# Performance work log

Measured on AMD Instinct MI355X. Metric: run time of the kernel, lower is better.

## Reference

```python
import jax, jax.numpy as jnp
import numpy as np

B, XD, PD, D, H = 512, 32768, 512, 64, 128  # batch, x_dim, proj_dim, latent_dim, per_dim_hidden
G1 = 1024  # gene projector hidden (hardcoded in module)


def _init(k, shape, fan_in):
    s = 1.0 / np.sqrt(fan_in)
    return jax.random.uniform(k, shape, jnp.float32, -s, s)


def setup_inputs() -> dict:
    key = jax.random.key(0)
    ks = jax.random.split(key, 16)
    return {
        "x": jax.random.normal(ks[0], (B, XD), jnp.float32),
        "z": jax.random.normal(ks[1], (B, D), jnp.float32),
        "perm": jax.random.permutation(ks[2], B).astype(jnp.int32),
        # shared gene projector
        "Wg1": _init(ks[3], (XD, G1), XD), "bg1": _init(ks[4], (G1,), XD),
        "Wg2": _init(ks[5], (G1, PD), G1), "bg2": _init(ks[6], (PD,), G1),
        # per-dimension 3-layer MLPs, stacked over D. Layer-1 weight [PD+1, H]
        # is split into the h-part Wh and the z-part Wz (last input column).
        "Wh": _init(ks[7], (D, PD, H), PD + 1),
        "Wz": _init(ks[8], (D, H), PD + 1),
        "b1": _init(ks[9], (D, H), PD + 1),
        "W2": _init(ks[10], (D, H, H), H), "b2": _init(ks[11], (D, H), H),
        "W3": _init(ks[12], (D, H), H), "b3": _init(ks[13], (D,), H),
    }


def reference(x, z, perm, Wg1, bg1, Wg2, bg2, Wh, Wz, b1, W2, b2, W3, b3):
    elu = jax.nn.elu
    # shared gene projector (eval mode: dropout = identity, no noise)
    h = elu(elu(x @ Wg1 + bg1) @ Wg2 + bg2)            # [B, PD]
    # batched layer-1 of all D per-dim nets; h-projection computed once and
    # reused for the marginal pass via permutation (h_shuffled = h[perm]).
    hWh = jnp.einsum('bp,dph->bdh', h, Wh)             # [B, D, H]
    zWz = z[:, :, None] * Wz[None]                     # [B, D, H]

    def head(a1_pre):
        a1 = elu(a1_pre)                               # [B, D, H]
        a2 = elu(jnp.einsum('bdh,dhk->bdk', a1, W2) + b2)
        return jnp.einsum('bdh,dh->bd', a2, W3) + b3   # [B, D] scalar scores

    joint_score = head(hWh + zWz + b1)                 # T(h, z_j)
    marg_score = head(hWh[perm] + zWz + b1)            # T(h_shuffled, z_j)

    emas = jnp.ones((D,), x.dtype)                     # buffer init = ones, eval: no update
    et = jnp.mean(jnp.exp(marg_score), axis=0)         # [D]
    mi = jnp.mean(joint_score, axis=0) - jnp.log(et / emas)
    return -jnp.mean(mi)
```

## Files before the change

### kernel.cpp

```cpp
#include <hip/hip_runtime.h>
#include <hip/hip_bf16.h>
#include <math.h>

#define B_  512
#define XD_ 32768
#define PD_ 512
#define D_  64
#define H_  128
#define G1_ 1024

typedef __attribute__((ext_vector_type(8))) short short8v;
typedef __attribute__((ext_vector_type(4))) float floatx4;

__device__ __forceinline__ float eluf(float v) { return v > 0.f ? v : expm1f(v); }

__device__ __forceinline__ void split8t(const float* c, short8v& h, short8v& l) {
    unsigned hu[8], lu[8];
    #pragma unroll
    for (int j = 0; j < 8; j++) {
        unsigned u = __float_as_uint(c[j]);
        hu[j] = u & 0xFFFF0000u;
        float res = c[j] - __uint_as_float(hu[j]);
        lu[j] = __float_as_uint(res);
    }
    uint4 hp, lp;
    hp.x = __builtin_amdgcn_perm(hu[1], hu[0], 0x07060302u);
    hp.y = __builtin_amdgcn_perm(hu[3], hu[2], 0x07060302u);
    hp.z = __builtin_amdgcn_perm(hu[5], hu[4], 0x07060302u);
    hp.w = __builtin_amdgcn_perm(hu[7], hu[6], 0x07060302u);
    lp.x = __builtin_amdgcn_perm(lu[1], lu[0], 0x07060302u);
    lp.y = __builtin_amdgcn_perm(lu[3], lu[2], 0x07060302u);
    lp.z = __builtin_amdgcn_perm(lu[5], lu[4], 0x07060302u);
    lp.w = __builtin_amdgcn_perm(lu[7], lu[6], 0x07060302u);
    h = __builtin_bit_cast(short8v, hp);
    l = __builtin_bit_cast(short8v, lp);
}

__global__ __launch_bounds__(256) void k_tr(const float* __restrict__ x,
                                            float* __restrict__ xT) {
    __shared__ float tile[64][65];
    const int k0 = blockIdx.x * 64;
    const int m0 = blockIdx.y * 64;
    const int t = threadIdx.x;
    const int tk = t & 63, tg = t >> 6;
    #pragma unroll
    for (int i = 0; i < 16; i++) {
        int r = tg * 16 + i;
        tile[r][tk] = x[(size_t)(m0 + r) * XD_ + k0 + tk];
    }
    __syncthreads();
    #pragma unroll
    for (int i = 0; i < 16; i++) {
        int r = tg * 16 + i;
        xT[(size_t)(k0 + r) * B_ + m0 + tk] = tile[tk][r];
    }
}

__global__ __launch_bounds__(256, 2) void k_gemm1t(const float* __restrict__ xT,
                                                   const float* __restrict__ Wg1,
                                                   float* __restrict__ part,
                                                   int KS) {
    __shared__ ushort Ah[2][4 * 128 * 8], Al[2][4 * 128 * 8];
    __shared__ ushort Bh[2][4 * 128 * 8], Bl[2][4 * 128 * 8];
    const int nt = blockIdx.x, mt = blockIdx.y, ks = blockIdx.z;
    const int t = threadIdx.x;
    const int w = t >> 6, lane = t & 63;
    const int q = lane >> 4, l15 = lane & 15;
    const int wr = w >> 1, wc = w & 1;
    const int kbS = t >> 6, pr = t & 63;
    const int k0 = ks * KS;

    const float* Ag = xT + (size_t)(k0 + kbS * 8) * B_ + mt * 128 + pr * 2;
    const float* Bg = Wg1 + (size_t)(k0 + kbS * 8) * G1_ + nt * 128 + pr * 2;

    floatx4 acc[4][4];
    #pragma unroll
    for (int i = 0; i < 4; i++)
        #pragma unroll
        for (int j = 0; j < 4; j++) acc[i][j] = (floatx4){0.f, 0.f, 0.f, 0.f};

    float2 pa[8], pb[8];
    #pragma unroll
    for (int kk = 0; kk < 8; kk++) {
        pa[kk] = *(const float2*)(Ag + (size_t)kk * B_);
        pb[kk] = *(const float2*)(Bg + (size_t)kk * G1_);
    }

    auto stage = [&](int buf) {
        float a0[8], a1[8], c0[8], c1[8];
        #pragma unroll
        for (int kk = 0; kk < 8; kk++) {
            a0[kk] = pa[kk].x; a1[kk] = pa[kk].y;
            c0[kk] = pb[kk].x; c1[kk] = pb[kk].y;
        }
        short8v ah0, al0, ah1, al1, bh0, bl0, bh1, bl1;
        split8t(a0, ah0, al0); split8t(a1, ah1, al1);
        split8t(c0, bh0, bl0); split8t(c1, bh1, bl1);
        int n0 = pr * 2;
        int ia0 = (kbS * 128 + (n0 ^ kbS)) * 8;
        int ia1 = (kbS * 128 + ((n0 + 1) ^ kbS)) * 8;
        *(short8v*)&Ah[buf][ia0] = ah0; *(short8v*)&Al[buf][ia0] = al0;
        *(short8v*)&Ah[buf][ia1] = ah1; *(short8v*)&Al[buf][ia1] = al1;
        *(short8v*)&Bh[buf][ia0] = bh0; *(short8v*)&Bl[buf][ia0] = bl0;
        *(short8v*)&Bh[buf][ia1] = bh1; *(short8v*)&Bl[buf][ia1] = bl1;
    };

    auto mma = [&](int buf) {
        short8v af[4], alf[4], bf[4], blf[4];
        #pragma unroll
        for (int i = 0; i < 4; i++) {
            int m = wr * 64 + i * 16 + l15;
            int idx = (q * 128 + (m ^ q)) * 8;
            af[i]  = *(const short8v*)&Ah[buf][idx];
            alf[i] = *(const short8v*)&Al[buf][idx];
        }
        #pragma unroll
        for (int j = 0; j < 4; j++) {
            int n = wc * 64 + j * 16 + l15;
            int idx = (q * 128 + (n ^ q)) * 8;
            bf[j]  = *(const short8v*)&Bh[buf][idx];
            blf[j] = *(const short8v*)&Bl[buf][idx];
        }
        #pragma unroll
        for (int i = 0; i < 4; i++)
            #pragma unroll
            for (int j = 0; j < 4; j++) {
                acc[i][j] = __builtin_amdgcn_mfma_f32_16x16x32_bf16(af[i],  bf[j],  acc[i][j], 0, 0, 0);
                acc[i][j] = __builtin_amdgcn_mfma_f32_16x16x32_bf16(af[i],  blf[j], acc[i][j], 0, 0, 0);
                acc[i][j] = __builtin_amdgcn_mfma_f32_16x16x32_bf16(alf[i], bf[j],  acc[i][j], 0, 0, 0);
            }
    };

    stage(0);
    #pragma unroll
    for (int kk = 0; kk < 8; kk++) {
        pa[kk] = *(const float2*)(Ag + (size_t)(32 + kk) * B_);
        pb[kk] = *(const float2*)(Bg + (size_t)(32 + kk) * G1_);
    }
    asm volatile("s_waitcnt lgkmcnt(0)" ::: "memory");
    __builtin_amdgcn_s_barrier();

    const int NT = KS >> 5;
    for (int it = 0; it < NT - 1; it++) {
        const int cur = it & 1;
        stage(cur ^ 1);
        if (it + 2 < NT) {
            #pragma unroll
            for (int kk = 0; kk < 8; kk++) {
                pa[kk] = *(const float2*)(Ag + (size_t)((it + 2) * 32 + kk) * B_);
                pb[kk] = *(const float2*)(Bg + (size_t)((it + 2) * 32 + kk) * G1_);
            }
        }
        mma(cur);
        asm volatile("s_waitcnt lgkmcnt(0)" ::: "memory");
        __builtin_amdgcn_s_barrier();
    }
    mma((NT - 1) & 1);

    float* P = part + (size_t)ks * (B_ * G1_) + (size_t)(mt * 128) * G1_ + nt * 128;
    #pragma unroll
    for (int i = 0; i < 4; i++)
        #pragma unroll
        for (int j = 0; j < 4; j++) {
            int col = wc * 64 + j * 16 + l15;
            #pragma unroll
            for (int r = 0; r < 4; r++) {
                int row = wr * 64 + i * 16 + q * 4 + r;
                P[(size_t)row * G1_ + col] = acc[i][j][r];
            }
        }
}

__global__ __launch_bounds__(256, 2) void k_gemm1m(const float* __restrict__ x,
                                                   const float* __restrict__ Wg1,
                                                   float* __restrict__ part,
                                                   int KS) {
    __shared__ ushort Ah[4 * 128 * 8], Al[4 * 128 * 8];
    __shared__ ushort Bh[4 * 128 * 8], Bl[4 * 128 * 8];
    const int nt = blockIdx.x, mt = blockIdx.y, ks = blockIdx.z;
    const int t = threadIdx.x;
    const int w = t >> 6, lane = t & 63;
    const int q = lane >> 4, l15 = lane & 15;
    const int wr = w >> 1, wc = w & 1;
    const int kbB = t >> 6, nb = t & 63;
    const int mA = t & 127, kbA = t >> 7;
    const int k0 = ks * KS;

    const float* Ag = x + (size_t)(mt * 128 + mA) * XD_ + k0 + kbA * 8;
    const float* Bg = Wg1 + (size_t)(k0 + kbB * 8) * G1_ + nt * 128 + nb * 2;

    floatx4 acc[4][4];
    #pragma unroll
    for (int i = 0; i < 4; i++)
        #pragma unroll
        for (int j = 0; j < 4; j++) acc[i][j] = (floatx4){0.f, 0.f, 0.f, 0.f};

    float4 pa0 = *(const float4*)(Ag);
    float4 pa1 = *(const float4*)(Ag + 4);
    float4 pa2 = *(const float4*)(Ag + 16);
    float4 pa3 = *(const float4*)(Ag + 20);
    float2 pb[8];
    #pragma unroll
    for (int kk = 0; kk < 8; kk++) pb[kk] = *(const float2*)(Bg + (size_t)kk * G1_);

    for (int kt = 0; kt < KS; kt += 32) {
        float cA0[8] = {pa0.x, pa0.y, pa0.z, pa0.w, pa1.x, pa1.y, pa1.z, pa1.w};
        float cA1[8] = {pa2.x, pa2.y, pa2.z, pa2.w, pa3.x, pa3.y, pa3.z, pa3.w};
        float c0[8], c1[8];
        #pragma unroll
        for (int kk = 0; kk < 8; kk++) { c0[kk] = pb[kk].x; c1[kk] = pb[kk].y; }
        short8v ah0, al0, ah1, al1, bh0, bl0, bh1, bl1;
        split8t(cA0, ah0, al0);
        split8t(cA1, ah1, al1);
        split8t(c0, bh0, bl0);
        split8t(c1, bh1, bl1);
        if (kt + 32 < KS) {
            pa0 = *(const float4*)(Ag + kt + 32);
            pa1 = *(const float4*)(Ag + kt + 36);
            pa2 = *(const float4*)(Ag + kt + 48);
            pa3 = *(const float4*)(Ag + kt + 52);
            const float* p = Bg + (size_t)(kt + 32) * G1_;
            #pragma unroll
            for (int kk = 0; kk < 8; kk++) pb[kk] = *(const float2*)(p + (size_t)kk * G1_);
        }
        {
            int ia0 = (kbA * 128 + (mA ^ kbA)) * 8;
            int ia1 = ((kbA + 2) * 128 + (mA ^ (kbA + 2))) * 8;
            *(short8v*)&Ah[ia0] = ah0; *(short8v*)&Al[ia0] = al0;
            *(short8v*)&Ah[ia1] = ah1; *(short8v*)&Al[ia1] = al1;
            int n0i = nb * 2;
            int i0 = (kbB * 128 + (n0i ^ kbB)) * 8;
            int i1 = (kbB * 128 + ((n0i + 1) ^ kbB)) * 8;
            *(short8v*)&Bh[i0] = bh0; *(short8v*)&Bl[i0] = bl0;
            *(short8v*)&Bh[i1] = bh1; *(short8v*)&Bl[i1] = bl1;
        }
        __syncthreads();
        short8v af[4], alf[4], bf[4], blf[4];
        #pragma unroll
        for (int i = 0; i < 4; i++) {
            int m = wr * 64 + i * 16 + l15;
            int idx = (q * 128 + (m ^ q)) * 8;
            af[i]  = *(const short8v*)&Ah[idx];
            alf[i] = *(const short8v*)&Al[idx];
        }
        #pragma unroll
        for (int j = 0; j < 4; j++) {
            int n = wc * 64 + j * 16 + l15;
            int idx = (q * 128 + (n ^ q)) * 8;
            bf[j]  = *(const short8v*)&Bh[idx];
            blf[j] = *(const short8v*)&Bl[idx];
        }
        #pragma unroll
        for (int i = 0; i < 4; i++)
            #pragma unroll
            for (int j = 0; j < 4; j++) {
                acc[i][j] = __builtin_amdgcn_mfma_f32_16x16x32_bf16(af[i],  bf[j],  acc[i][j], 0, 0, 0);
                acc[i][j] = __builtin_amdgcn_mfma_f32_16x16x32_bf16(af[i],  blf[j], acc[i][j], 0, 0, 0);
                acc[i][j] = __builtin_amdgcn_mfma_f32_16x16x32_bf16(alf[i], bf[j],  acc[i][j], 0, 0, 0);
            }
        __syncthreads();
    }
    float* P = part + (size_t)ks * (B_ * G1_) + (size_t)(mt * 128) * G1_ + nt * 128;
    #pragma unroll
    for (int i = 0; i < 4; i++)
        #pragma unroll
        for (int j = 0; j < 4; j++) {
            int col = wc * 64 + j * 16 + l15;
            #pragma unroll
            for (int r = 0; r < 4; r++) {
                int row = wr * 64 + i * 16 + q * 4 + r;
                P[(size_t)row * G1_ + col] = acc[i][j][r];
            }
        }
}

__global__ __launch_bounds__(256) void k_red1(const float* __restrict__ part,
                                              const float* __restrict__ bg1,
                                              ushort* __restrict__ Gh,
                                              ushort* __restrict__ Gl,
                                              int nparts) {
    int idx = (blockIdx.x * 256 + threadIdx.x) * 8;
    const int S = B_ * G1_;
    float c[8] = {};
    for (int k = 0; k < nparts; k++) {
        const float* p = part + (size_t)k * S + idx;
        float4 v0 = *(const float4*)p, v1 = *(const float4*)(p + 4);
        c[0] += v0.x; c[1] += v0.y; c[2] += v0.z; c[3] += v0.w;
        c[4] += v1.x; c[5] += v1.y; c[6] += v1.z; c[7] += v1.w;
    }
    int cb = idx & (G1_ - 1);
    float4 b0 = *(const float4*)(bg1 + cb), b1v = *(const float4*)(bg1 + cb + 4);
    c[0] = eluf(c[0] + b0.x); c[1] = eluf(c[1] + b0.y);
    c[2] = eluf(c[2] + b0.z); c[3] = eluf(c[3] + b0.w);
    c[4] = eluf(c[4] + b1v.x); c[5] = eluf(c[5] + b1v.y);
    c[6] = eluf(c[6] + b1v.z); c[7] = eluf(c[7] + b1v.w);
    short8v h, l; split8t(c, h, l);
    *(short8v*)(Gh + idx) = h;
    *(short8v*)(Gl + idx) = l;
}

__global__ __launch_bounds__(256, 2) void k_gemm2m(const ushort* __restrict__ Gh,
                                                   const ushort* __restrict__ Gl,
                                                   const float* __restrict__ Wg2,
                                                   float* __restrict__ part2) {
    __shared__ ushort Ah[4 * 64 * 8], Al[4 * 64 * 8];
    __shared__ ushort Bh[4 * 64 * 8], Bl[4 * 64 * 8];
    const int nt = blockIdx.x, mt = blockIdx.y, ks = blockIdx.z;
    const int t = threadIdx.x;
    const int w = t >> 6, lane = t & 63;
    const int q = lane >> 4, l15 = lane & 15;
    const int kb = (t >> 4) & 3;
    const int rb = (t & 15) | (w << 4);
    const int k0 = ks * 128;

    const int cB = t & 63, g = t >> 6;

    floatx4 acc[4];
    #pragma unroll
    for (int i = 0; i < 4; i++) acc[i] = (floatx4){0.f, 0.f, 0.f, 0.f};

    for (int kt = 0; kt < 128; kt += 32) {
        {
            const ushort* pH = Gh + (size_t)(mt * 64 + rb) * G1_ + k0 + kt + kb * 8;
            const ushort* pL = Gl + (size_t)(mt * 64 + rb) * G1_ + k0 + kt + kb * 8;
            uint4 vh = *(const uint4*)pH;
            uint4 vl = *(const uint4*)pL;
            int idx = (kb * 64 + (rb ^ kb)) * 8;
            *(uint4*)&Ah[idx] = vh;
            *(uint4*)&Al[idx] = vl;
        }
        {
            float c[8];
            const float* p = Wg2 + (size_t)(k0 + kt + g * 8) * PD_ + nt * 64 + cB;
            #pragma unroll
            for (int kk = 0; kk < 8; kk++) c[kk] = p[(size_t)kk * PD_];
            short8v h, l; split8t(c, h, l);
            int idx = (g * 64 + (cB ^ g)) * 8;
            *(short8v*)&Bh[idx] = h;
            *(short8v*)&Bl[idx] = l;
        }
        __syncthreads();
        short8v af[4], alf[4], bf, blf;
        #pragma unroll
        for (int i = 0; i < 4; i++) {
            int m = i * 16 + l15;
            int idx = (q * 64 + (m ^ q)) * 8;
            af[i]  = *(const short8v*)&Ah[idx];
            alf[i] = *(const short8v*)&Al[idx];
        }
        {
            int n = w * 16 + l15;
            int idx = (q * 64 + (n ^ q)) * 8;
            bf  = *(const short8v*)&Bh[idx];
            blf = *(const short8v*)&Bl[idx];
        }
        #pragma unroll
        for (int i = 0; i < 4; i++) {
            acc[i] = __builtin_amdgcn_mfma_f32_16x16x32_bf16(af[i],  bf,  acc[i], 0, 0, 0);
            acc[i] = __builtin_amdgcn_mfma_f32_16x16x32_bf16(af[i],  blf, acc[i], 0, 0, 0);
            acc[i] = __builtin_amdgcn_mfma_f32_16x16x32_bf16(alf[i], bf,  acc[i], 0, 0, 0);
        }
        __syncthreads();
    }
    float* P = part2 + (size_t)ks * (B_ * PD_) + (size_t)(mt * 64) * PD_ + nt * 64;
    #pragma unroll
    for (int i = 0; i < 4; i++) {
        int col = w * 16 + l15;
        #pragma unroll
        for (int r = 0; r < 4; r++) {
            int row = i * 16 + q * 4 + r;
            P[(size_t)row * PD_ + col] = acc[i][r];
        }
    }
}

__global__ __launch_bounds__(256) void k_red2(const float* __restrict__ part2,
                                              const float* __restrict__ bg2,
                                              ushort* __restrict__ hh,
                                              ushort* __restrict__ hl) {
    int idx = (blockIdx.x * 256 + threadIdx.x) * 8;
    const int S = B_ * PD_;
    float c[8] = {};
    #pragma unroll
    for (int k = 0; k < 8; k++) {
        const float* p = part2 + (size_t)k * S + idx;
        float4 v0 = *(const float4*)p, v1 = *(const float4*)(p + 4);
        c[0] += v0.x; c[1] += v0.y; c[2] += v0.z; c[3] += v0.w;
        c[4] += v1.x; c[5] += v1.y; c[6] += v1.z; c[7] += v1.w;
    }
    int cb = idx & (PD_ - 1);
    float4 b0 = *(const float4*)(bg2 + cb), b1v = *(const float4*)(bg2 + cb + 4);
    c[0] = eluf(c[0] + b0.x); c[1] = eluf(c[1] + b0.y);
    c[2] = eluf(c[2] + b0.z); c[3] = eluf(c[3] + b0.w);
    c[4] = eluf(c[4] + b1v.x); c[5] = eluf(c[5] + b1v.y);
    c[6] = eluf(c[6] + b1v.z); c[7] = eluf(c[7] + b1v.w);
    short8v h, l; split8t(c, h, l);
    *(short8v*)(hh + idx) = h;
    *(short8v*)(hl + idx) = l;
}

__global__ __launch_bounds__(256, 2) void k_hwh_m(const ushort* __restrict__ hh,
                                                  const ushort* __restrict__ hl,
                                                  const float* __restrict__ Wh,
                                                  float* __restrict__ hWh) {
    __shared__ ushort Ah[4 * 64 * 8], Al[4 * 64 * 8];
    __shared__ ushort Bh[4 * 128 * 8], Bl[4 * 128 * 8];
    const int d = blockIdx.x, mt = blockIdx.y;
    const int t = threadIdx.x;
    const int w = t >> 6, lane = t & 63;
    const int q = lane >> 4, l15 = lane & 15;
    const int kb = (t >> 4) & 3;
    const int rb = (t & 15) | (w << 4);

    const ushort* AgH = hh + (size_t)(mt * 64 + rb) * PD_ + kb * 8;
    const ushort* AgL = hl + (size_t)(mt * 64 + rb) * PD_ + kb * 8;
    const float* Bg = Wh + (size_t)d * (PD_ * H_) + (size_t)(kb * 8) * H_ + rb * 2;

    floatx4 acc[4][2];
    #pragma unroll
    for (int i = 0; i < 4; i++)
        #pragma unroll
        for (int j = 0; j < 2; j++) acc[i][j] = (floatx4){0.f, 0.f, 0.f, 0.f};

    uint4 pah = *(const uint4*)(AgH);
    uint4 pal = *(const uint4*)(AgL);
    float2 pb[8];
    #pragma unroll
    for (int kk = 0; kk < 8; kk++) pb[kk] = *(const float2*)(Bg + (size_t)kk * H_);

    for (int kt = 0; kt < PD_; kt += 32) {
        float c0[8], c1[8];
        #pragma unroll
        for (int kk = 0; kk < 8; kk++) { c0[kk] = pb[kk].x; c1[kk] = pb[kk].y; }
        short8v bh0, bl0, bh1, bl1;
        split8t(c0, bh0, bl0);
        split8t(c1, bh1, bl1);
        uint4 ah = pah, al = pal;
        if (kt + 32 < PD_) {
            pah = *(const uint4*)(AgH + kt + 32);
            pal = *(const uint4*)(AgL + kt + 32);
            const float* p = Bg + (size_t)(kt + 32) * H_;
            #pragma unroll
            for (int kk = 0; kk < 8; kk++) pb[kk] = *(const float2*)(p + (size_t)kk * H_);
        }
        {
            int idx = (kb * 64 + (rb ^ kb)) * 8;
            *(uint4*)&Ah[idx] = ah;
            *(uint4*)&Al[idx] = al;
            int n0i = rb * 2;
            int i0 = (kb * 128 + (n0i ^ kb)) * 8;
            int i1 = (kb * 128 + ((n0i + 1) ^ kb)) * 8;
            *(short8v*)&Bh[i0] = bh0; *(short8v*)&Bl[i0] = bl0;
            *(short8v*)&Bh[i1] = bh1; *(short8v*)&Bl[i1] = bl1;
        }
        __syncthreads();
        short8v af[4], alf[4], bf[2], blf[2];
        #pragma unroll
        for (int i = 0; i < 4; i++) {
            int m = i * 16 + l15;
            int idx = (q * 64 + (m ^ q)) * 8;
            af[i]  = *(const short8v*)&Ah[idx];
            alf[i] = *(const short8v*)&Al[idx];
        }
        #pragma unroll
        for (int j = 0; j < 2; j++) {
            int n = w * 32 + j * 16 + l15;
            int idx = (q * 128 + (n ^ q)) * 8;
            bf[j]  = *(const short8v*)&Bh[idx];
            blf[j] = *(const short8v*)&Bl[idx];
        }
        #pragma unroll
        for (int i = 0; i < 4; i++)
            #pragma unroll
            for (int j = 0; j < 2; j++) {
                acc[i][j] = __builtin_amdgcn_mfma_f32_16x16x32_bf16(af[i],  bf[j],  acc[i][j], 0, 0, 0);
                acc[i][j] = __builtin_amdgcn_mfma_f32_16x16x32_bf16(af[i],  blf[j], acc[i][j], 0, 0, 0);
                acc[i][j] = __builtin_amdgcn_mfma_f32_16x16x32_bf16(alf[i], bf[j],  acc[i][j], 0, 0, 0);
            }
        __syncthreads();
    }
    #pragma unroll
    for (int i = 0; i < 4; i++)
        #pragma unroll
        for (int j = 0; j < 2; j++) {
            int col = w * 32 + j * 16 + l15;
            #pragma unroll
            for (int r = 0; r < 4; r++) {
                int row = i * 16 + q * 4 + r;
                int b = mt * 64 + row;
                hWh[(size_t)b * (D_ * H_) + d * H_ + col] = acc[i][j][r];
            }
        }
}

__global__ __launch_bounds__(256, 2) void k_heads(const float* __restrict__ hWh,
                                                  const float* __restrict__ z,
                                                  const int* __restrict__ perm,
                                                  const float* __restrict__ Wz,
                                                  const float* __restrict__ b1,
                                                  const float* __restrict__ W2,
                                                  const float* __restrict__ b2,
                                                  const float* __restrict__ W3,
                                                  const float* __restrict__ b3,
                                                  float* __restrict__ jpart,
                                                  float* __restrict__ epart) {
    const int chunk = blockIdx.x;
    const int d = blockIdx.y;
    const int t = threadIdx.x;
    const int b0 = chunk * 64;
    __shared__ ushort A1h[16 * 64 * 8];
    __shared__ ushort A1l[16 * 64 * 8];
    __shared__ float  BS[4096];
    ushort* Bh = (ushort*)BS;
    ushort* Bl = Bh + 4096;
    float*  sred = BS;

    const int w = t >> 6, lane = t & 63;
    const int q = lane >> 4, l15 = lane & 15;
    const int kb = (t >> 4) & 3;
    const int rb = (t & 15) | (w << 4);

    const float* W2d = W2 + (size_t)d * H_ * H_;
    const float* Wzd = Wz + d * H_;
    const float* b1d = b1 + d * H_;
    const float* b2d = b2 + d * H_;
    const float* W3d = W3 + d * H_;

    float result0 = 0.f, result1 = 0.f;
    for (int pass = 0; pass < 2; pass++) {
        {
            int i = t >> 2;
            int kt = t & 3;
            int h0 = kt * 32;
            int bb = b0 + i;
            int src = (pass == 0) ? bb : perm[bb];
            float zv = z[bb * D_ + d];
            const float* hrow = hWh + (size_t)src * (D_ * H_) + d * H_;
            #pragma unroll
            for (int kq = 0; kq < 4; kq++) {
                float c[8];
                int kbase = h0 + kq * 8;
                float4 v0 = *(const float4*)(hrow + kbase);
                float4 v1 = *(const float4*)(hrow + kbase + 4);
                float4 w0 = *(const float4*)(Wzd + kbase);
                float4 w1 = *(const float4*)(Wzd + kbase + 4);
                float4 x0 = *(const float4*)(b1d + kbase);
                float4 x1 = *(const float4*)(b1d + kbase + 4);
                c[0] = eluf(v0.x + zv * w0.x + x0.x);
                c[1] = eluf(v0.y + zv * w0.y + x0.y);
                c[2] = eluf(v0.z + zv * w0.z + x0.z);
                c[3] = eluf(v0.w + zv * w0.w + x0.w);
                c[4] = eluf(v1.x + zv * w1.x + x1.x);
                c[5] = eluf(v1.y + zv * w1.y + x1.y);
                c[6] = eluf(v1.z + zv * w1.z + x1.z);
                c[7] = eluf(v1.w + zv * w1.w + x1.w);
                short8v hv, lv; split8t(c, hv, lv);
                int idx = ((kt * 4 + kq) * 64 + (i ^ kq)) * 8;
                *(short8v*)&A1h[idx] = hv;
                *(short8v*)&A1l[idx] = lv;
            }
        }
        __syncthreads();
        floatx4 acc[4][2];
        #pragma unroll
        for (int i = 0; i < 4; i++)
            #pragma unroll
            for (int j = 0; j < 2; j++) acc[i][j] = (floatx4){0.f, 0.f, 0.f, 0.f};
        for (int kt2 = 0; kt2 < 4; kt2++) {
            {
                float c0[8], c1[8];
                const float* p = W2d + (size_t)(kt2 * 32 + kb * 8) * H_ + rb * 2;
                #pragma unroll
                for (int kk = 0; kk < 8; kk++) {
                    float2 v = *(const float2*)(p + (size_t)kk * H_);
                    c0[kk] = v.x; c1[kk] = v.y;
                }
                short8v h0v, l0v, h1v, l1v;
                split8t(c0, h0v, l0v);
                split8t(c1, h1v, l1v);
                int n0i = rb * 2;
                int i0 = (kb * 128 + (n0i ^ kb)) * 8;
                int i1 = (kb * 128 + ((n0i + 1) ^ kb)) * 8;
                *(short8v*)&Bh[i0] = h0v; *(short8v*)&Bl[i0] = l0v;
                *(short8v*)&Bh[i1] = h1v; *(short8v*)&Bl[i1] = l1v;
            }
            __syncthreads();
            short8v af[4], alf[4], bf[2], blf[2];
            #pragma unroll
            for (int i = 0; i < 4; i++) {
                int m = i * 16 + l15;
                int idx = ((kt2 * 4 + q) * 64 + (m ^ q)) * 8;
                af[i]  = *(const short8v*)&A1h[idx];
                alf[i] = *(const short8v*)&A1l[idx];
            }
            #pragma unroll
            for (int j = 0; j < 2; j++) {
                int n = w * 32 + j * 16 + l15;
                int idx = (q * 128 + (n ^ q)) * 8;
                bf[j]  = *(const short8v*)&Bh[idx];
                blf[j] = *(const short8v*)&Bl[idx];
            }
            #pragma unroll
            for (int i = 0; i < 4; i++)
                #pragma unroll
                for (int j = 0; j < 2; j++) {
                    acc[i][j] = __builtin_amdgcn_mfma_f32_16x16x32_bf16(af[i],  bf[j],  acc[i][j], 0, 0, 0);
                    acc[i][j] = __builtin_amdgcn_mfma_f32_16x16x32_bf16(af[i],  blf[j], acc[i][j], 0, 0, 0);
                    acc[i][j] = __builtin_amdgcn_mfma_f32_16x16x32_bf16(alf[i], bf[j],  acc[i][j], 0, 0, 0);
                }
            __syncthreads();
        }
        #pragma unroll
        for (int i = 0; i < 4; i++) {
            #pragma unroll
            for (int r = 0; r < 4; r++) {
                int b = i * 16 + q * 4 + r;
                float s = 0.f;
                #pragma unroll
                for (int j = 0; j < 2; j++) {
                    int col = w * 32 + j * 16 + l15;
                    float a2v = eluf(acc[i][j][r] + b2d[col]);
                    s = fmaf(a2v, W3d[col], s);
                }
                sred[b * 64 + w * 16 + l15] = s;
            }
        }
        __syncthreads();
        float val = 0.f;
        if (t < 64) {
            float s = b3[d];
            const float4* row = (const float4*)&sred[t * 64];
            #pragma unroll
            for (int c = 0; c < 16; c++) {
                float4 v = row[c];
                s += v.x + v.y + v.z + v.w;
            }
            val = (pass == 0) ? s : expf(s);
            #pragma unroll
            for (int off = 32; off > 0; off >>= 1)
                val += __shfl_down(val, off, 64);
        }
        if (t == 0) { if (pass == 0) result0 = val; else result1 = val; }
        __syncthreads();
    }
    if (t == 0) {
        jpart[d * 8 + chunk] = result0;
        epart[d * 8 + chunk] = result1;
    }
}

__global__ void k_final(const float* __restrict__ jpart,
                        const float* __restrict__ epart,
                        float* __restrict__ out) {
    int t = threadIdx.x;
    float mj = 0.f, me = 0.f;
    #pragma unroll
    for (int c = 0; c < 8; c++) { mj += jpart[t * 8 + c]; me += epart[t * 8 + c]; }
    mj *= (1.f / 512.f);
    me *= (1.f / 512.f);
    float mi = mj - logf(me);
    #pragma unroll
    for (int off = 32; off > 0; off >>= 1) mi += __shfl_down(mi, off, 64);
    if (t == 0) out[0] = -mi * (1.f / 64.f);
}

extern "C" void kernel_launch(void* const* d_in, const int* in_sizes, int n_in,
                              void* d_out, int out_size, void* d_ws, size_t ws_size,
                              hipStream_t stream) {
    const float* x   = (const float*)d_in[0];
    const float* z   = (const float*)d_in[1];
    const int*  perm = (const int*)d_in[2];
    const float* Wg1 = (const float*)d_in[3];
    const float* bg1 = (const float*)d_in[4];
    const float* Wg2 = (const float*)d_in[5];
    const float* bg2 = (const float*)d_in[6];
    const float* Wh  = (const float*)d_in[7];
    const float* Wz  = (const float*)d_in[8];
    const float* b1  = (const float*)d_in[9];
    const float* W2  = (const float*)d_in[10];
    const float* b2  = (const float*)d_in[11];
    const float* W3  = (const float*)d_in[12];
    const float* b3  = (const float*)d_in[13];
    float* out = (float*)d_out;

    char* base = (char*)d_ws;
    const size_t PART_SLICE = (size_t)B_ * G1_ * sizeof(float);

    const size_t NEW_NEED = 16 * PART_SLICE + 67108864ull + 2097152 + 1048576 + 4096;

    if (ws_size >= NEW_NEED) {
        float* part  = (float*)base;
        float* xT    = (float*)(base + 33554432);
        float* hWh   = (float*)base;
        float* part2 = (float*)(base + 16777216);
        ushort* Gh   = (ushort*)(base + 100663296);
        ushort* Gl   = Gh + 524288;
        ushort* hh   = (ushort*)(base + 102760448);
        ushort* hl   = hh + 262144;
        float* jpart = (float*)(base + 103809024);
        float* epart = jpart + 512;

        k_tr<<<dim3(512, 8), 256, 0, stream>>>(x, xT);
        k_gemm1t<<<dim3(8, 4, 16), 256, 0, stream>>>(xT, Wg1, part, XD_ / 16);
        k_red1<<<256, 256, 0, stream>>>(part, bg1, Gh, Gl, 16);
        k_gemm2m<<<dim3(8, 8, 8), 256, 0, stream>>>(Gh, Gl, Wg2, part2);
        k_red2<<<128, 256, 0, stream>>>(part2, bg2, hh, hl);
        k_hwh_m<<<dim3(64, 8), 256, 0, stream>>>(hh, hl, Wh, hWh);
        k_heads<<<dim3(8, 64), 256, 0, stream>>>(hWh, z, perm, Wz, b1, W2, b2, W3, b3,
                                                 jpart, epart);
        k_final<<<1, 64, 0, stream>>>(jpart, epart, out);
    } else {
        int nks = (ws_size >= (size_t)32 * PART_SLICE + 3145728 + 4096) ? 32 : 16;
        const int KS = XD_ / nks;
        const size_t partBytes = (size_t)nks * PART_SLICE;

        float* part  = (float*)base;
        float* hWh   = (float*)base;
        float* part2 = (float*)(base + 16777216);
        ushort* Gh   = (ushort*)(base + partBytes);
        ushort* Gl   = Gh + 524288;
        ushort* hh   = (ushort*)(base + partBytes + 2097152);
        ushort* hl   = hh + 262144;
        float* jpart = (float*)(base + partBytes + 3145728);
        float* epart = jpart + 512;

        k_gemm1m<<<dim3(8, 4, nks), 256, 0, stream>>>(x, Wg1, part, KS);
        k_red1<<<256, 256, 0, stream>>>(part, bg1, Gh, Gl, nks);
        k_gemm2m<<<dim3(8, 8, 8), 256, 0, stream>>>(Gh, Gl, Wg2, part2);
        k_red2<<<128, 256, 0, stream>>>(part2, bg2, hh, hl);
        k_hwh_m<<<dim3(64, 8), 256, 0, stream>>>(hh, hl, Wh, hWh);
        k_heads<<<dim3(8, 64), 256, 0, stream>>>(hWh, z, perm, Wz, b1, W2, b2, W3, b3,
                                                 jpart, epart);
        k_final<<<1, 64, 0, stream>>>(jpart, epart, out);
    }
}
```

Before: 432.9 us.

## Pre-split x into bf16 hi/lo tiles in transpose; parallelize head passes over grid z

The transpose kernel now converts x directly into bf16 hi/lo halves stored in a k-blocked layout that the first GEMM can copy straight into shared memory. This removes the per-tile split work and the strided float2 loads from the GEMM inner loop and replaces the fp32 transpose through LDS. Separately, the heads kernel runs the joint and marginal passes as separate blocks via a third grid dimension, doubling parallelism at the cost of reloading W2 per pass.

```diff
diff --git a/kernel.cpp b/kernel.cpp
--- a/kernel.cpp
+++ b/kernel.cpp
@@ -36,27 +36,29 @@
     l = __builtin_bit_cast(short8v, lp);
 }
 
-__global__ __launch_bounds__(256) void k_tr(const float* __restrict__ x,
-                                            float* __restrict__ xT) {
-    __shared__ float tile[64][65];
+__global__ __launch_bounds__(256) void k_trs(const float* __restrict__ x,
+                                             ushort* __restrict__ xh,
+                                             ushort* __restrict__ xl) {
     const int k0 = blockIdx.x * 64;
     const int m0 = blockIdx.y * 64;
     const int t = threadIdx.x;
-    const int tk = t & 63, tg = t >> 6;
-    #pragma unroll
-    for (int i = 0; i < 16; i++) {
-        int r = tg * 16 + i;
-        tile[r][tk] = x[(size_t)(m0 + r) * XD_ + k0 + tk];
-    }
-    __syncthreads();
-    #pragma unroll
-    for (int i = 0; i < 16; i++) {
-        int r = tg * 16 + i;
-        xT[(size_t)(k0 + r) * B_ + m0 + tk] = tile[tk][r];
-    }
-}
-
-__global__ __launch_bounds__(256, 2) void k_gemm1t(const float* __restrict__ xT,
+    const int m = t & 63;
+    const int kq = t >> 6;
+    #pragma unroll
+    for (int i = 0; i < 2; i++) {
+        int kg = kq * 2 + i;
+        const float* p = x + (size_t)(m0 + m) * XD_ + k0 + kg * 8;
+        float4 v0 = *(const float4*)p, v1 = *(const float4*)(p + 4);
+        float c[8] = {v0.x, v0.y, v0.z, v0.w, v1.x, v1.y, v1.z, v1.w};
+        short8v h, l; split8t(c, h, l);
+        size_t off = ((size_t)((k0 >> 3) + kg) * B_ + m0 + m) * 8;
+        *(short8v*)(xh + off) = h;
+        *(short8v*)(xl + off) = l;
+    }
+}
+
+__global__ __launch_bounds__(256, 2) void k_gemm1t(const ushort* __restrict__ xh,
+                                                   const ushort* __restrict__ xl,
                                                    const float* __restrict__ Wg1,
                                                    float* __restrict__ part,
                                                    int KS) {
@@ -67,11 +69,13 @@
     const int w = t >> 6, lane = t & 63;
     const int q = lane >> 4, l15 = lane & 15;
     const int wr = w >> 1, wc = w & 1;
-    const int kbS = t >> 6, pr = t & 63;
+    const int q4 = t >> 6, pr = t & 63;
     const int k0 = ks * KS;
 
-    const float* Ag = xT + (size_t)(k0 + kbS * 8) * B_ + mt * 128 + pr * 2;
-    const float* Bg = Wg1 + (size_t)(k0 + kbS * 8) * G1_ + nt * 128 + pr * 2;
+    const size_t aoff = (((size_t)(k0 >> 3) + q4) * B_ + mt * 128 + pr) * 8;
+    const ushort* Agh = xh + aoff;
+    const ushort* Agl = xl + aoff;
+    const float*  Bg  = Wg1 + (size_t)(k0 + q4 * 8) * G1_ + nt * 128 + pr * 2;
 
     floatx4 acc[4][4];
     #pragma unroll
@@ -79,30 +83,36 @@
         #pragma unroll
         for (int j = 0; j < 4; j++) acc[i][j] = (floatx4){0.f, 0.f, 0.f, 0.f};
 
-    float2 pa[8], pb[8];
-    #pragma unroll
-    for (int kk = 0; kk < 8; kk++) {
-        pa[kk] = *(const float2*)(Ag + (size_t)kk * B_);
-        pb[kk] = *(const float2*)(Bg + (size_t)kk * G1_);
-    }
+    uint4 pAh0, pAh1, pAl0, pAl1;
+    float2 pb[8];
+
+    auto loadT = [&](int kt) {
+        size_t o = (size_t)kt * B_;
+        pAh0 = *(const uint4*)(Agh + o);
+        pAh1 = *(const uint4*)(Agh + o + 512);
+        pAl0 = *(const uint4*)(Agl + o);
+        pAl1 = *(const uint4*)(Agl + o + 512);
+        const float* p = Bg + (size_t)kt * G1_;
+        #pragma unroll
+        for (int kk = 0; kk < 8; kk++) pb[kk] = *(const float2*)(p + (size_t)kk * G1_);
+    };
 
     auto stage = [&](int buf) {
-        float a0[8], a1[8], c0[8], c1[8];
-        #pragma unroll
-        for (int kk = 0; kk < 8; kk++) {
-            a0[kk] = pa[kk].x; a1[kk] = pa[kk].y;
-            c0[kk] = pb[kk].x; c1[kk] = pb[kk].y;
-        }
-        short8v ah0, al0, ah1, al1, bh0, bl0, bh1, bl1;
-        split8t(a0, ah0, al0); split8t(a1, ah1, al1);
+        float c0[8], c1[8];
+        #pragma unroll
+        for (int kk = 0; kk < 8; kk++) { c0[kk] = pb[kk].x; c1[kk] = pb[kk].y; }
+        short8v bh0, bl0, bh1, bl1;
         split8t(c0, bh0, bl0); split8t(c1, bh1, bl1);
         int n0 = pr * 2;
-        int ia0 = (kbS * 128 + (n0 ^ kbS)) * 8;
-        int ia1 = (kbS * 128 + ((n0 + 1) ^ kbS)) * 8;
-        *(short8v*)&Ah[buf][ia0] = ah0; *(short8v*)&Al[buf][ia0] = al0;
-        *(short8v*)&Ah[buf][ia1] = ah1; *(short8v*)&Al[buf][ia1] = al1;
-        *(short8v*)&Bh[buf][ia0] = bh0; *(short8v*)&Bl[buf][ia0] = bl0;
-        *(short8v*)&Bh[buf][ia1] = bh1; *(short8v*)&Bl[buf][ia1] = bl1;
+        int i0 = (q4 * 128 + (n0 ^ q4)) * 8;
+        int i1 = (q4 * 128 + ((n0 + 1) ^ q4)) * 8;
+        *(short8v*)&Bh[buf][i0] = bh0; *(short8v*)&Bl[buf][i0] = bl0;
+        *(short8v*)&Bh[buf][i1] = bh1; *(short8v*)&Bl[buf][i1] = bl1;
+        int ia0 = (q4 * 128 + (pr ^ q4)) * 8;
+        *(uint4*)&Ah[buf][ia0] = pAh0;
+        *(uint4*)&Al[buf][ia0] = pAl0;
+        *(uint4*)&Ah[buf][ia0 + 512] = pAh1;
+        *(uint4*)&Al[buf][ia0 + 512] = pAl1;
     };
 
     auto mma = [&](int buf) {
@@ -131,12 +141,9 @@
             }
     };
 
+    loadT(0);
     stage(0);
-    #pragma unroll
-    for (int kk = 0; kk < 8; kk++) {
-        pa[kk] = *(const float2*)(Ag + (size_t)(32 + kk) * B_);
-        pb[kk] = *(const float2*)(Bg + (size_t)(32 + kk) * G1_);
-    }
+    loadT(32);
     asm volatile("s_waitcnt lgkmcnt(0)" ::: "memory");
     __builtin_amdgcn_s_barrier();
 
@@ -144,13 +151,7 @@
     for (int it = 0; it < NT - 1; it++) {
         const int cur = it & 1;
         stage(cur ^ 1);
-        if (it + 2 < NT) {
-            #pragma unroll
-            for (int kk = 0; kk < 8; kk++) {
-                pa[kk] = *(const float2*)(Ag + (size_t)((it + 2) * 32 + kk) * B_);
-                pb[kk] = *(const float2*)(Bg + (size_t)((it + 2) * 32 + kk) * G1_);
-            }
-        }
+        if (it + 2 < NT) loadT((it + 2) * 32);
         mma(cur);
         asm volatile("s_waitcnt lgkmcnt(0)" ::: "memory");
         __builtin_amdgcn_s_barrier();
@@ -506,6 +507,7 @@
                                                   float* __restrict__ epart) {
     const int chunk = blockIdx.x;
     const int d = blockIdx.y;
+    const int pass = blockIdx.z;
     const int t = threadIdx.x;
     const int b0 = chunk * 64;
     __shared__ ushort A1h[16 * 64 * 8];
@@ -526,126 +528,121 @@
     const float* b2d = b2 + d * H_;
     const float* W3d = W3 + d * H_;
 
-    float result0 = 0.f, result1 = 0.f;
-    for (int pass = 0; pass < 2; pass++) {
+    {
+        int i = t >> 2;
+        int kt = t & 3;
+        int h0 = kt * 32;
+        int bb = b0 + i;
+        int src = (pass == 0) ? bb : perm[bb];
+        float zv = z[bb * D_ + d];
+        const float* hrow = hWh + (size_t)src * (D_ * H_) + d * H_;
+        #pragma unroll
+        for (int kq = 0; kq < 4; kq++) {
+            float c[8];
+            int kbase = h0 + kq * 8;
+            float4 v0 = *(const float4*)(hrow + kbase);
+            float4 v1 = *(const float4*)(hrow + kbase + 4);
+            float4 w0 = *(const float4*)(Wzd + kbase);
+            float4 w1 = *(const float4*)(Wzd + kbase + 4);
+            float4 x0 = *(const float4*)(b1d + kbase);
+            float4 x1 = *(const float4*)(b1d + kbase + 4);
+            c[0] = eluf(v0.x + zv * w0.x + x0.x);
+            c[1] = eluf(v0.y + zv * w0.y + x0.y);
+            c[2] = eluf(v0.z + zv * w0.z + x0.z);
+            c[3] = eluf(v0.w + zv * w0.w + x0.w);
+            c[4] = eluf(v1.x + zv * w1.x + x1.x);
+            c[5] = eluf(v1.y + zv * w1.y + x1.y);
+            c[6] = eluf(v1.z + zv * w1.z + x1.z);
+            c[7] = eluf(v1.w + zv * w1.w + x1.w);
+            short8v hv, lv; split8t(c, hv, lv);
+            int idx = ((kt * 4 + kq) * 64 + (i ^ kq)) * 8;
+            *(short8v*)&A1h[idx] = hv;
+            *(short8v*)&A1l[idx] = lv;
+        }
+    }
+    __syncthreads();
+    floatx4 acc[4][2];
+    #pragma unroll
+    for (int i = 0; i < 4; i++)
+        #pragma unroll
+        for (int j = 0; j < 2; j++) acc[i][j] = (floatx4){0.f, 0.f, 0.f, 0.f};
+    for (int kt2 = 0; kt2 < 4; kt2++) {
         {
-            int i = t >> 2;
-            int kt = t & 3;
-            int h0 = kt * 32;
-            int bb = b0 + i;
-            int src = (pass == 0) ? bb : perm[bb];
-            float zv = z[bb * D_ + d];
-            const float* hrow = hWh + (size_t)src * (D_ * H_) + d * H_;
-            #pragma unroll
-            for (int kq = 0; kq < 4; kq++) {
-                float c[8];
-                int kbase = h0 + kq * 8;
-                float4 v0 = *(const float4*)(hrow + kbase);
-                float4 v1 = *(const float4*)(hrow + kbase + 4);
-                float4 w0 = *(const float4*)(Wzd + kbase);
-                float4 w1 = *(const float4*)(Wzd + kbase + 4);
-                float4 x0 = *(const float4*)(b1d + kbase);
-                float4 x1 = *(const float4*)(b1d + kbase + 4);
-                c[0] = eluf(v0.x + zv * w0.x + x0.x);
-                c[1] = eluf(v0.y + zv * w0.y + x0.y);
-                c[2] = eluf(v0.z + zv * w0.z + x0.z);
-                c[3] = eluf(v0.w + zv * w0.w + x0.w);
-                c[4] = eluf(v1.x + zv * w1.x + x1.x);
-                c[5] = eluf(v1.y + zv * w1.y + x1.y);
-                c[6] = eluf(v1.z + zv * w1.z + x1.z);
-                c[7] = eluf(v1.w + zv * w1.w + x1.w);
-                short8v hv, lv; split8t(c, hv, lv);
-                int idx = ((kt * 4 + kq) * 64 + (i ^ kq)) * 8;
-                *(short8v*)&A1h[idx] = hv;
-                *(short8v*)&A1l[idx] = lv;
-            }
+            float c0[8], c1[8];
+            const float* p = W2d + (size_t)(kt2 * 32 + kb * 8) * H_ + rb * 2;
+            #pragma unroll
+            for (int kk = 0; kk < 8; kk++) {
+                float2 v = *(const float2*)(p + (size_t)kk * H_);
+                c0[kk] = v.x; c1[kk] = v.y;
+            }
+            short8v h0v, l0v, h1v, l1v;
+            split8t(c0, h0v, l0v);
+            split8t(c1, h1v, l1v);
+            int n0i = rb * 2;
+            int i0 = (kb * 128 + (n0i ^ kb)) * 8;
+            int i1 = (kb * 128 + ((n0i + 1) ^ kb)) * 8;
+            *(short8v*)&Bh[i0] = h0v; *(short8v*)&Bl[i0] = l0v;
+            *(short8v*)&Bh[i1] = h1v; *(short8v*)&Bl[i1] = l1v;
         }
         __syncthreads();
-        floatx4 acc[4][2];
+        short8v af[4], alf[4], bf[2], blf[2];
+        #pragma unroll
+        for (int i = 0; i < 4; i++) {
+            int m = i * 16 + l15;
+            int idx = ((kt2 * 4 + q) * 64 + (m ^ q)) * 8;
+            af[i]  = *(const short8v*)&A1h[idx];
+            alf[i] = *(const short8v*)&A1l[idx];
+        }
+        #pragma unroll
+        for (int j = 0; j < 2; j++) {
+            int n = w * 32 + j * 16 + l15;
+            int idx = (q * 128 + (n ^ q)) * 8;
+            bf[j]  = *(const short8v*)&Bh[idx];
+            blf[j] = *(const short8v*)&Bl[idx];
+        }
         #pragma unroll
         for (int i = 0; i < 4; i++)
             #pragma unroll
-            for (int j = 0; j < 2; j++) acc[i][j] = (floatx4){0.f, 0.f, 0.f, 0.f};
-        for (int kt2 = 0; kt2 < 4; kt2++) {
-            {
-                float c0[8], c1[8];
-                const float* p = W2d + (size_t)(kt2 * 32 + kb * 8) * H_ + rb * 2;
-                #pragma unroll
-                for (int kk = 0; kk < 8; kk++) {
-                    float2 v = *(const float2*)(p + (size_t)kk * H_);
-                    c0[kk] = v.x; c1[kk] = v.y;
-                }
-                short8v h0v, l0v, h1v, l1v;
-                split8t(c0, h0v, l0v);
-                split8t(c1, h1v, l1v);
-                int n0i = rb * 2;
-                int i0 = (kb * 128 + (n0i ^ kb)) * 8;
-                int i1 = (kb * 128 + ((n0i + 1) ^ kb)) * 8;
-                *(short8v*)&Bh[i0] = h0v; *(short8v*)&Bl[i0] = l0v;
-                *(short8v*)&Bh[i1] = h1v; *(short8v*)&Bl[i1] = l1v;
-            }
-            __syncthreads();
-            short8v af[4], alf[4], bf[2], blf[2];
-            #pragma unroll
-            for (int i = 0; i < 4; i++) {
-                int m = i * 16 + l15;
-                int idx = ((kt2 * 4 + q) * 64 + (m ^ q)) * 8;
-                af[i]  = *(const short8v*)&A1h[idx];
-                alf[i] = *(const short8v*)&A1l[idx];
-            }
-            #pragma unroll
             for (int j = 0; j < 2; j++) {
-                int n = w * 32 + j * 16 + l15;
-                int idx = (q * 128 + (n ^ q)) * 8;
-                bf[j]  = *(const short8v*)&Bh[idx];
-                blf[j] = *(const short8v*)&Bl[idx];
-            }
-            #pragma unroll
-            for (int i = 0; i < 4; i++)
-                #pragma unroll
-                for (int j = 0; j < 2; j++) {
-                    acc[i][j] = __builtin_amdgcn_mfma_f32_16x16x32_bf16(af[i],  bf[j],  acc[i][j], 0, 0, 0);
-                    acc[i][j] = __builtin_amdgcn_mfma_f32_16x16x32_bf16(af[i],  blf[j], acc[i][j], 0, 0, 0);
-                    acc[i][j] = __builtin_amdgcn_mfma_f32_16x16x32_bf16(alf[i], bf[j],  acc[i][j], 0, 0, 0);
-                }
-            __syncthreads();
-        }
-        #pragma unroll
-        for (int i = 0; i < 4; i++) {
-            #pragma unroll
-            for (int r = 0; r < 4; r++) {
-                int b = i * 16 + q * 4 + r;
-                float s = 0.f;
-                #pragma unroll
-                for (int j = 0; j < 2; j++) {
-                    int col = w * 32 + j * 16 + l15;
-                    float a2v = eluf(acc[i][j][r] + b2d[col]);
-                    s = fmaf(a2v, W3d[col], s);
-                }
-                sred[b * 64 + w * 16 + l15] = s;
-            }
-        }
+                acc[i][j] = __builtin_amdgcn_mfma_f32_16x16x32_bf16(af[i],  bf[j],  acc[i][j], 0, 0, 0);
+                acc[i][j] = __builtin_amdgcn_mfma_f32_16x16x32_bf16(af[i],  blf[j], acc[i][j], 0, 0, 0);
+                acc[i][j] = __builtin_amdgcn_mfma_f32_16x16x32_bf16(alf[i], bf[j],  acc[i][j], 0, 0, 0);
+            }
         __syncthreads();
-        float val = 0.f;
-        if (t < 64) {
-            float s = b3[d];
-            const float4* row = (const float4*)&sred[t * 64];
-            #pragma unroll
-            for (int c = 0; c < 16; c++) {
-                float4 v = row[c];
-                s += v.x + v.y + v.z + v.w;
-            }
-            val = (pass == 0) ? s : expf(s);
-            #pragma unroll
-            for (int off = 32; off > 0; off >>= 1)
-                val += __shfl_down(val, off, 64);
-        }
-        if (t == 0) { if (pass == 0) result0 = val; else result1 = val; }
-        __syncthreads();
+    }
+    #pragma unroll
+    for (int i = 0; i < 4; i++) {
+        #pragma unroll
+        for (int r = 0; r < 4; r++) {
+            int b = i * 16 + q * 4 + r;
+            float s = 0.f;
+            #pragma unroll
+            for (int j = 0; j < 2; j++) {
+                int col = w * 32 + j * 16 + l15;
+                float a2v = eluf(acc[i][j][r] + b2d[col]);
+                s = fmaf(a2v, W3d[col], s);
+            }
+            sred[b * 64 + w * 16 + l15] = s;
+        }
+    }
+    __syncthreads();
+    float val = 0.f;
+    if (t < 64) {
+        float s = b3[d];
+        const float4* row = (const float4*)&sred[t * 64];
+        #pragma unroll
+        for (int c = 0; c < 16; c++) {
+            float4 v = row[c];
+            s += v.x + v.y + v.z + v.w;
+        }
+        val = (pass == 0) ? s : expf(s);
+        #pragma unroll
+        for (int off = 32; off > 0; off >>= 1)
+            val += __shfl_down(val, off, 64);
     }
     if (t == 0) {
-        jpart[d * 8 + chunk] = result0;
-        epart[d * 8 + chunk] = result1;
+        if (pass == 0) jpart[d * 8 + chunk] = val;
+        else           epart[d * 8 + chunk] = val;
     }
 }
 
@@ -690,7 +687,8 @@
 
     if (ws_size >= NEW_NEED) {
         float* part  = (float*)base;
-        float* xT    = (float*)(base + 33554432);
+        ushort* xh   = (ushort*)(base + 33554432);
+        ushort* xl   = (ushort*)(base + 67108864);
         float* hWh   = (float*)base;
         float* part2 = (float*)(base + 16777216);
         ushort* Gh   = (ushort*)(base + 100663296);
@@ -700,14 +698,14 @@
         float* jpart = (float*)(base + 103809024);
         float* epart = jpart + 512;
 
-        k_tr<<<dim3(512, 8), 256, 0, stream>>>(x, xT);
-        k_gemm1t<<<dim3(8, 4, 16), 256, 0, stream>>>(xT, Wg1, part, XD_ / 16);
+        k_trs<<<dim3(512, 8), 256, 0, stream>>>(x, xh, xl);
+        k_gemm1t<<<dim3(8, 4, 16), 256, 0, stream>>>(xh, xl, Wg1, part, XD_ / 16);
         k_red1<<<256, 256, 0, stream>>>(part, bg1, Gh, Gl, 16);
         k_gemm2m<<<dim3(8, 8, 8), 256, 0, stream>>>(Gh, Gl, Wg2, part2);
         k_red2<<<128, 256, 0, stream>>>(part2, bg2, hh, hl);
         k_hwh_m<<<dim3(64, 8), 256, 0, stream>>>(hh, hl, Wh, hWh);
-        k_heads<<<dim3(8, 64), 256, 0, stream>>>(hWh, z, perm, Wz, b1, W2, b2, W3, b3,
-                                                 jpart, epart);
+        k_heads<<<dim3(8, 64, 2), 256, 0, stream>>>(hWh, z, perm, Wz, b1, W2, b2, W3, b3,
+                                                    jpart, epart);
         k_final<<<1, 64, 0, stream>>>(jpart, epart, out);
     } else {
         int nks = (ws_size >= (size_t)32 * PART_SLICE + 3145728 + 4096) ? 32 : 16;
@@ -729,8 +727,8 @@
         k_gemm2m<<<dim3(8, 8, 8), 256, 0, stream>>>(Gh, Gl, Wg2, part2);
         k_red2<<<128, 256, 0, stream>>>(part2, bg2, hh, hl);
         k_hwh_m<<<dim3(64, 8), 256, 0, stream>>>(hh, hl, Wh, hWh);
-        k_heads<<<dim3(8, 64), 256, 0, stream>>>(hWh, z, perm, Wz, b1, W2, b2, W3, b3,
-                                                 jpart, epart);
+        k_heads<<<dim3(8, 64, 2), 256, 0, stream>>>(hWh, z, perm, Wz, b1, W2, b2, W3, b3,
+                                                    jpart, epart);
         k_final<<<1, 64, 0, stream>>>(jpart, epart, out);
     }
 }
```

After: 427.8 us. About the same (-1.2%).
